# Kernel tuning notes

Hardware: AMD Instinct MI355X
Metric: run time of the kernel (lower is better)

The kernel has to match this reference:

```python
import jax, jax.numpy as jnp
import numpy as np


def setup_inputs() -> dict:
    key = jax.random.key(0)
    ks = jax.random.split(key, 6)
    B, C, S, E = 8, 16, 512, 256
    wscale = (2.0 / (E + E)) ** 0.5  # xavier_normal for [E, E] fan_in=fan_out=E
    return {
        "query": jax.random.normal(ks[0], (B, C, S, E), dtype=jnp.float32),
        "key": jax.random.normal(ks[1], (B, C, S, E), dtype=jnp.float32),
        "value": jax.random.normal(ks[2], (B, C, S, E), dtype=jnp.float32),
        "q_proj_weight": jax.random.normal(ks[3], (C, E, E), dtype=jnp.float32) * wscale,
        "k_proj_weight": jax.random.normal(ks[4], (C, E, E), dtype=jnp.float32) * wscale,
        "v_proj_weight": jax.random.normal(ks[5], (C, E, E), dtype=jnp.float32) * wscale,
        "q_proj_bias": jnp.zeros((C, 1, E), dtype=jnp.float32),
        "k_proj_bias": jnp.zeros((C, 1, E), dtype=jnp.float32),
        "v_proj_bias": jnp.zeros((C, 1, E), dtype=jnp.float32),
    }


def reference(query, key, value, q_proj_weight, k_proj_weight, v_proj_weight,
              q_proj_bias, k_proj_bias, v_proj_bias):
    E = query.shape[-1]
    # Per-cycle projection + bias + ReLU.  b=batch, c=cycle, s/t=seq, e/f=embed
    q = jax.nn.relu(jnp.einsum("bcse,cef->bcsf", query, q_proj_weight) + q_proj_bias)
    k = jax.nn.relu(jnp.einsum("bcse,cef->bcsf", key, k_proj_weight) + k_proj_bias)
    v = jax.nn.relu(jnp.einsum("bcse,cef->bcsf", value, v_proj_weight) + v_proj_bias)
    q = q * (float(E) ** -0.5)
    attn = jax.nn.softmax(jnp.einsum("bcse,bcte->bcst", q, k), axis=-1)
    out = jnp.einsum("bcst,bcte->bcse", attn, v)
    return out
```

## Files before the change

### kernel.cpp

```cpp
#include <hip/hip_runtime.h>

constexpr int BATCH = 8;
constexpr int CYC   = 16;
constexpr int SEQ   = 512;
constexpr int EMB   = 256;

typedef __attribute__((ext_vector_type(8))) short bf16x8;
typedef __attribute__((ext_vector_type(4))) float f32x4;

__device__ __forceinline__ unsigned short f2bf(float x) {
    unsigned int u = __float_as_uint(x);
    u += 0x7fffu + ((u >> 16) & 1u);
    return (unsigned short)(u >> 16);
}
__device__ __forceinline__ unsigned int pk2(float lo, float hi) {
    return (unsigned int)f2bf(lo) | ((unsigned int)f2bf(hi) << 16);
}

__device__ __forceinline__ f32x4 mfma16(bf16x8 a, bf16x8 b, f32x4 c) {
    return __builtin_amdgcn_mfma_f32_16x16x32_bf16(a, b, c, 0, 0, 0);
}

__device__ __forceinline__ void gll16(const unsigned short* g, unsigned short* l) {
    __builtin_amdgcn_global_load_lds(
        (const __attribute__((address_space(1))) void*)g,
        (__attribute__((address_space(3))) void*)l, 16, 0, 0);
}

__global__ __launch_bounds__(256) void wt_kernel(const float* __restrict__ W,
                                                 unsigned short* __restrict__ Wt) {
    __shared__ float tile[64][65];
    const int c  = blockIdx.z;
    const int e0 = blockIdx.x * 64;
    const int f0 = blockIdx.y * 64;
    const float* Wc = W + (size_t)c * EMB * EMB;
    unsigned short* Wtc = Wt + (size_t)c * EMB * EMB;
    const int t = threadIdx.x;
    {
        const int er = t >> 4;
        const int fc = (t & 15) * 4;
        for (int i = 0; i < 4; ++i) {
            const float4 v = *(const float4*)(Wc + (size_t)(e0 + er + i * 16) * EMB + f0 + fc);
            tile[er + i * 16][fc + 0] = v.x;
            tile[er + i * 16][fc + 1] = v.y;
            tile[er + i * 16][fc + 2] = v.z;
            tile[er + i * 16][fc + 3] = v.w;
        }
    }
    __syncthreads();
    {
        const int fr = t >> 4;
        const int ec = (t & 15) * 4;
        for (int i = 0; i < 4; ++i) {
            const int f = fr + i * 16;
            ushort4 o;
            o.x = f2bf(tile[ec + 0][f]);
            o.y = f2bf(tile[ec + 1][f]);
            o.z = f2bf(tile[ec + 2][f]);
            o.w = f2bf(tile[ec + 3][f]);
            *(ushort4*)(Wtc + (size_t)(f0 + f) * EMB + e0 + ec) = o;
        }
    }
}

__global__ __launch_bounds__(256) void proj_kernel(
    const float* __restrict__ X, const unsigned short* __restrict__ Wt,
    const float* __restrict__ bias, unsigned short* __restrict__ Y,
    const float scale, const int transposeOut)
{
    __shared__ unsigned short smem[10752];
    unsigned short* As = smem;
    unsigned short* Bs = smem + 2560;
    const int bc = blockIdx.x;
    const int c  = bc & (CYC - 1);
    const int m0 = blockIdx.y * 64;
    const float* Xb = X + (size_t)bc * SEQ * EMB;
    const unsigned short* Wc = Wt + (size_t)c * EMB * EMB;
    const float* bb = bias + (size_t)c * EMB;
    unsigned short* Yb = Y + (size_t)bc * SEQ * EMB;

    const int tid  = threadIdx.x;
    const int lane = tid & 63, w = tid >> 6;
    const int ln   = lane & 15, quad = lane >> 4;
    const int wu   = __builtin_amdgcn_readfirstlane(w);

    const int arow = tid >> 2;
    const int acol = (tid & 3) * 8;
    const int brow = lane >> 2;
    const int gch  = (lane & 3) ^ ((lane >> 3) & 3);
    const int bslot = quad ^ ((ln >> 1) & 3);

    f32x4 acc[4][4];
    for (int i = 0; i < 4; ++i)
        for (int j = 0; j < 4; ++j) acc[i][j] = (f32x4){0.f, 0.f, 0.f, 0.f};

    for (int kk = 0; kk < 8; ++kk) {
        const int k0 = kk * 32;
        const float* ax = Xb + (size_t)(m0 + arow) * EMB + k0 + acol;
        const float4 a0 = *(const float4*)ax;
        const float4 a1 = *(const float4*)(ax + 4);
        int4 pk;
        pk.x = pk2(a0.x, a0.y); pk.y = pk2(a0.z, a0.w);
        pk.z = pk2(a1.x, a1.y); pk.w = pk2(a1.z, a1.w);
        *(int4*)&As[arow * 40 + acol] = pk;
        for (int j = 0; j < 4; ++j) {
            const int r = wu * 64 + j * 16 + brow;
            gll16(Wc + (size_t)r * EMB + k0 + gch * 8,
                  Bs + (size_t)(wu * 64 + j * 16) * 32);
        }
        __syncthreads();
        bf16x8 af[4], bfv[4];
        for (int i = 0; i < 4; ++i)
            af[i] = *(const bf16x8*)&As[(i * 16 + ln) * 40 + quad * 8];
        for (int j = 0; j < 4; ++j)
            bfv[j] = *(const bf16x8*)&Bs[(w * 64 + j * 16 + ln) * 32 + bslot * 8];
        for (int i = 0; i < 4; ++i)
            for (int j = 0; j < 4; ++j)
                acc[i][j] = mfma16(af[i], bfv[j], acc[i][j]);
        __syncthreads();
    }

    float bvj[4];
    for (int j = 0; j < 4; ++j) bvj[j] = bb[w * 64 + j * 16 + ln];

    if (!transposeOut) {
        unsigned short* ep = smem + w * 1152;
        for (int i = 0; i < 4; ++i) {
            for (int j = 0; j < 4; ++j)
                for (int r = 0; r < 4; ++r)
                    ep[(quad * 4 + r) * 72 + j * 16 + ln] =
                        f2bf(fmaxf(acc[i][j][r] + bvj[j], 0.f) * scale);
            __syncthreads();
            for (int h = 0; h < 2; ++h) {
                const int cid = lane + h * 64;
                const int row = cid >> 3, ch = cid & 7;
                *(bf16x8*)&Yb[(size_t)(m0 + i * 16 + row) * EMB + w * 64 + ch * 8] =
                    *(const bf16x8*)&ep[row * 72 + ch * 8];
            }
            __syncthreads();
        }
    } else {
        for (int j = 0; j < 4; ++j) {
            const int fg = w * 64 + j * 16 + ln;
            for (int i = 0; i < 4; ++i) {
                const int mb = m0 + i * 16 + quad * 4;
                ushort4 u;
                u.x = f2bf(fmaxf(acc[i][j][0] + bvj[j], 0.f) * scale);
                u.y = f2bf(fmaxf(acc[i][j][1] + bvj[j], 0.f) * scale);
                u.z = f2bf(fmaxf(acc[i][j][2] + bvj[j], 0.f) * scale);
                u.w = f2bf(fmaxf(acc[i][j][3] + bvj[j], 0.f) * scale);
                *(ushort4*)&Yb[(size_t)fg * SEQ + mb] = u;
            }
        }
    }
}

__global__ __launch_bounds__(256) void attn_kernel(
    const unsigned short* __restrict__ Qp, const unsigned short* __restrict__ Kp,
    const unsigned short* __restrict__ Vt, float* __restrict__ Out)
{
    __shared__ unsigned short Ks[32][264];
    __shared__ unsigned short Vs[256][40];
    __shared__ unsigned short Ps[64][40];
    const int bc = blockIdx.x;
    const int qt = blockIdx.y;
    const unsigned short* Qb = Qp + (size_t)bc * SEQ * EMB;
    const unsigned short* Kb = Kp + (size_t)bc * SEQ * EMB;
    const unsigned short* Vb = Vt + (size_t)bc * SEQ * EMB;
    float* Ob = Out + (size_t)bc * SEQ * EMB;

    const int tid  = threadIdx.x;
    const int lane = tid & 63, w = tid >> 6;
    const int ln   = lane & 15, quad = lane >> 4;

    bf16x8 qf[8];
    const int qrow = qt * 64 + w * 16 + ln;
    for (int ke = 0; ke < 8; ++ke)
        qf[ke] = *(const bf16x8*)(Qb + (size_t)qrow * EMB + ke * 32 + quad * 8);

    f32x4 of[16];
    for (int n = 0; n < 16; ++n) of[n] = (f32x4){0.f, 0.f, 0.f, 0.f};
    float lsum[4] = {0.f, 0.f, 0.f, 0.f};

    for (int tt = 0; tt < 16; ++tt) {
        const int t0 = tt * 32;
        for (int i = 0; i < 4; ++i) {
            const int idx = tid + i * 256;
            const int r = idx >> 5, c8 = (idx & 31) * 8;
            *(bf16x8*)&Ks[r][c8] = *(const bf16x8*)(Kb + (size_t)(t0 + r) * EMB + c8);
        }
        for (int i = 0; i < 4; ++i) {
            const int idx = tid + i * 256;
            const int e = idx >> 2, c8 = (idx & 3) * 8;
            *(bf16x8*)&Vs[e][c8] = *(const bf16x8*)(Vb + (size_t)e * SEQ + t0 + c8);
        }
        __syncthreads();

        f32x4 sf0 = (f32x4){0.f,0.f,0.f,0.f}, sf1 = (f32x4){0.f,0.f,0.f,0.f};
        for (int ke = 0; ke < 8; ++ke) {
            bf16x8 b0 = *(const bf16x8*)&Ks[ln][ke * 32 + quad * 8];
            bf16x8 b1 = *(const bf16x8*)&Ks[16 + ln][ke * 32 + quad * 8];
            sf0 = mfma16(qf[ke], b0, sf0);
            sf1 = mfma16(qf[ke], b1, sf1);
        }

        float p0[4], p1[4];
        for (int r = 0; r < 4; ++r) {
            p0[r] = __expf(sf0[r]);
            p1[r] = __expf(sf1[r]);
            lsum[r] += p0[r] + p1[r];
        }
        for (int r = 0; r < 4; ++r) {
            Ps[w * 16 + quad * 4 + r][ln]      = f2bf(p0[r]);
            Ps[w * 16 + quad * 4 + r][16 + ln] = f2bf(p1[r]);
        }
        __syncthreads();

        bf16x8 af = *(const bf16x8*)&Ps[w * 16 + ln][quad * 8];
        for (int n = 0; n < 16; ++n) {
            bf16x8 bv = *(const bf16x8*)&Vs[n * 16 + ln][quad * 8];
            of[n] = mfma16(af, bv, of[n]);
        }
        __syncthreads();
    }

    for (int off = 1; off < 16; off <<= 1)
        for (int r = 0; r < 4; ++r)
            lsum[r] += __shfl_xor(lsum[r], off, 64);
    float inv[4];
    for (int r = 0; r < 4; ++r) inv[r] = 1.0f / lsum[r];
    const int mbase = qt * 64 + w * 16 + quad * 4;
    for (int n = 0; n < 16; ++n)
        for (int r = 0; r < 4; ++r)
            Ob[(size_t)(mbase + r) * EMB + n * 16 + ln] = of[n][r] * inv[r];
}

extern "C" void kernel_launch(void* const* d_in, const int* in_sizes, int n_in,
                              void* d_out, int out_size, void* d_ws, size_t ws_size,
                              hipStream_t stream) {
    const float* query = (const float*)d_in[0];
    const float* key_  = (const float*)d_in[1];
    const float* value = (const float*)d_in[2];
    const float* wq = (const float*)d_in[3];
    const float* wk = (const float*)d_in[4];
    const float* wv = (const float*)d_in[5];
    const float* bq = (const float*)d_in[6];
    const float* bk = (const float*)d_in[7];
    const float* bv = (const float*)d_in[8];
    float* out = (float*)d_out;

    char* ws = (char*)d_ws;
    const size_t wsz = (size_t)CYC * EMB * EMB * sizeof(unsigned short);
    const size_t psz = (size_t)BATCH * CYC * SEQ * EMB * sizeof(unsigned short);
    unsigned short* Wtq = (unsigned short*)(ws);
    unsigned short* Wtk = (unsigned short*)(ws + wsz);
    unsigned short* Wtv = (unsigned short*)(ws + 2 * wsz);
    unsigned short* Qp  = (unsigned short*)(ws + 3 * wsz);
    unsigned short* Kp  = (unsigned short*)(ws + 3 * wsz + psz);
    unsigned short* Vtp = (unsigned short*)(ws + 3 * wsz + 2 * psz);

    const dim3 tb(256);
    wt_kernel<<<dim3(4, 4, CYC), tb, 0, stream>>>(wq, Wtq);
    wt_kernel<<<dim3(4, 4, CYC), tb, 0, stream>>>(wk, Wtk);
    wt_kernel<<<dim3(4, 4, CYC), tb, 0, stream>>>(wv, Wtv);

    const dim3 pg(BATCH * CYC, SEQ / 64);
    proj_kernel<<<pg, tb, 0, stream>>>(query, Wtq, bq, Qp, 0.0625f, 0);
    proj_kernel<<<pg, tb, 0, stream>>>(key_,  Wtk, bk, Kp, 1.0f, 0);
    proj_kernel<<<pg, tb, 0, stream>>>(value, Wtv, bv, Vtp, 1.0f, 1);

    attn_kernel<<<dim3(BATCH * CYC, SEQ / 64), tb, 0, stream>>>(Qp, Kp, Vtp, out);
}
```

Before: 351.3 us.

## Merge Q/K/V launches, double-buffer LDS staging, read K directly in attention

The three weight-transpose launches and the three projection launches each become one launch, with blockIdx.z choosing among Q, K and V. The projection kernel now double-buffers fp32 activations and bf16 weights in LDS via async global-to-LDS loads and converts to bf16 after reading from LDS. The attention kernel drops the K tile from LDS and reads K fragments straight from global, while V tiles are double-buffered with async loads and explicit waitcnt/barriers. The aim is to cut launch overhead and hide load latency behind MFMA work, at the cost of more LDS per block and uncoalesced direct K reads.

Result: slower. 411.5 us (+17.1%).

```diff
diff --git a/kernel.cpp b/kernel.cpp
--- a/kernel.cpp
+++ b/kernel.cpp
@@ -16,21 +16,27 @@
 __device__ __forceinline__ unsigned int pk2(float lo, float hi) {
     return (unsigned int)f2bf(lo) | ((unsigned int)f2bf(hi) << 16);
 }
-
 __device__ __forceinline__ f32x4 mfma16(bf16x8 a, bf16x8 b, f32x4 c) {
     return __builtin_amdgcn_mfma_f32_16x16x32_bf16(a, b, c, 0, 0, 0);
 }
-
-__device__ __forceinline__ void gll16(const unsigned short* g, unsigned short* l) {
+__device__ __forceinline__ void gll16(const void* g, void* l) {
     __builtin_amdgcn_global_load_lds(
         (const __attribute__((address_space(1))) void*)g,
         (__attribute__((address_space(3))) void*)l, 16, 0, 0);
 }
-
-__global__ __launch_bounds__(256) void wt_kernel(const float* __restrict__ W,
-                                                 unsigned short* __restrict__ Wt) {
+union BCast { int4 i; bf16x8 v; };
+
+__global__ __launch_bounds__(256) void wt_kernel(
+    const float* __restrict__ Wq, const float* __restrict__ Wk,
+    const float* __restrict__ Wv,
+    unsigned short* __restrict__ Tq, unsigned short* __restrict__ Tk,
+    unsigned short* __restrict__ Tv)
+{
     __shared__ float tile[64][65];
-    const int c  = blockIdx.z;
+    const int z = blockIdx.z;
+    const int which = z >> 4, c = z & 15;
+    const float* W = which == 0 ? Wq : which == 1 ? Wk : Wv;
+    unsigned short* Wt = which == 0 ? Tq : which == 1 ? Tk : Tv;
     const int e0 = blockIdx.x * 64;
     const int f0 = blockIdx.y * 64;
     const float* Wc = W + (size_t)c * EMB * EMB;
@@ -63,14 +69,26 @@
     }
 }
 
-__global__ __launch_bounds__(256) void proj_kernel(
-    const float* __restrict__ X, const unsigned short* __restrict__ Wt,
-    const float* __restrict__ bias, unsigned short* __restrict__ Y,
-    const float scale, const int transposeOut)
+__global__ __launch_bounds__(256, 3) void proj_kernel(
+    const float* __restrict__ Xq, const float* __restrict__ Xk,
+    const float* __restrict__ Xv,
+    const unsigned short* __restrict__ Wq, const unsigned short* __restrict__ Wk,
+    const unsigned short* __restrict__ Wv,
+    const float* __restrict__ Bq, const float* __restrict__ Bk,
+    const float* __restrict__ Bv,
+    unsigned short* __restrict__ Yq, unsigned short* __restrict__ Yk,
+    unsigned short* __restrict__ Yv)
 {
-    __shared__ unsigned short smem[10752];
-    unsigned short* As = smem;
-    unsigned short* Bs = smem + 2560;
+    __shared__ float          As[2][64 * 32];
+    __shared__ unsigned short Bs[2][256 * 32];
+
+    const int z = blockIdx.z;
+    const float* X = z == 0 ? Xq : z == 1 ? Xk : Xv;
+    const unsigned short* Wt = z == 0 ? Wq : z == 1 ? Wk : Wv;
+    const float* bias = z == 0 ? Bq : z == 1 ? Bk : Bv;
+    unsigned short* Y = z == 0 ? Yq : z == 1 ? Yk : Yv;
+    const float scale = z == 0 ? 0.0625f : 1.0f;
+
     const int bc = blockIdx.x;
     const int c  = bc & (CYC - 1);
     const int m0 = blockIdx.y * 64;
@@ -84,47 +102,77 @@
     const int ln   = lane & 15, quad = lane >> 4;
     const int wu   = __builtin_amdgcn_readfirstlane(w);
 
-    const int arow = tid >> 2;
-    const int acol = (tid & 3) * 8;
+    const int arow = lane >> 3;
+    const int achk = (lane & 7) ^ arow;
     const int brow = lane >> 2;
     const int gch  = (lane & 3) ^ ((lane >> 3) & 3);
+    const int s8    = ln & 7;
     const int bslot = quad ^ ((ln >> 1) & 3);
 
     f32x4 acc[4][4];
     for (int i = 0; i < 4; ++i)
         for (int j = 0; j < 4; ++j) acc[i][j] = (f32x4){0.f, 0.f, 0.f, 0.f};
 
+    auto stage = [&](int kk, int b) {
+        const int k0 = kk * 32;
+#pragma unroll
+        for (int j = 0; j < 2; ++j) {
+            const int r0 = wu * 16 + j * 8;
+            gll16(Xb + (size_t)(m0 + r0 + arow) * EMB + k0 + achk * 4,
+                  &As[b][r0 * 32]);
+        }
+#pragma unroll
+        for (int j = 0; j < 4; ++j) {
+            const int r0 = wu * 64 + j * 16;
+            gll16(Wc + (size_t)(r0 + brow) * EMB + k0 + gch * 8,
+                  &Bs[b][r0 * 32]);
+        }
+    };
+
+    stage(0, 0);
+#pragma unroll
     for (int kk = 0; kk < 8; ++kk) {
-        const int k0 = kk * 32;
-        const float* ax = Xb + (size_t)(m0 + arow) * EMB + k0 + acol;
-        const float4 a0 = *(const float4*)ax;
-        const float4 a1 = *(const float4*)(ax + 4);
-        int4 pk;
-        pk.x = pk2(a0.x, a0.y); pk.y = pk2(a0.z, a0.w);
-        pk.z = pk2(a1.x, a1.y); pk.w = pk2(a1.z, a1.w);
-        *(int4*)&As[arow * 40 + acol] = pk;
-        for (int j = 0; j < 4; ++j) {
-            const int r = wu * 64 + j * 16 + brow;
-            gll16(Wc + (size_t)r * EMB + k0 + gch * 8,
-                  Bs + (size_t)(wu * 64 + j * 16) * 32);
-        }
-        __syncthreads();
+        const int cur = kk & 1;
+        if (kk < 7) {
+            stage(kk + 1, cur ^ 1);
+            asm volatile("s_waitcnt vmcnt(6)" ::: "memory");
+        } else {
+            asm volatile("s_waitcnt vmcnt(0)" ::: "memory");
+        }
+        __builtin_amdgcn_s_barrier();
+        __builtin_amdgcn_sched_barrier(0);
+
         bf16x8 af[4], bfv[4];
+#pragma unroll
+        for (int i = 0; i < 4; ++i) {
+            const float* ar = &As[cur][(i * 16 + ln) * 32];
+            const float4 f0 = *(const float4*)(ar + ((2 * quad)     ^ s8) * 4);
+            const float4 f1 = *(const float4*)(ar + ((2 * quad + 1) ^ s8) * 4);
+            BCast u;
+            u.i.x = pk2(f0.x, f0.y); u.i.y = pk2(f0.z, f0.w);
+            u.i.z = pk2(f1.x, f1.y); u.i.w = pk2(f1.z, f1.w);
+            af[i] = u.v;
+        }
+#pragma unroll
+        for (int j = 0; j < 4; ++j)
+            bfv[j] = *(const bf16x8*)&Bs[cur][(w * 64 + j * 16 + ln) * 32 + bslot * 8];
+#pragma unroll
         for (int i = 0; i < 4; ++i)
-            af[i] = *(const bf16x8*)&As[(i * 16 + ln) * 40 + quad * 8];
-        for (int j = 0; j < 4; ++j)
-            bfv[j] = *(const bf16x8*)&Bs[(w * 64 + j * 16 + ln) * 32 + bslot * 8];
-        for (int i = 0; i < 4; ++i)
+#pragma unroll
             for (int j = 0; j < 4; ++j)
                 acc[i][j] = mfma16(af[i], bfv[j], acc[i][j]);
-        __syncthreads();
+
+        __builtin_amdgcn_sched_barrier(0);
+        asm volatile("s_waitcnt lgkmcnt(0)" ::: "memory");
+        __builtin_amdgcn_s_barrier();
     }
 
     float bvj[4];
+#pragma unroll
     for (int j = 0; j < 4; ++j) bvj[j] = bb[w * 64 + j * 16 + ln];
 
-    if (!transposeOut) {
-        unsigned short* ep = smem + w * 1152;
+    if (z != 2) {
+        unsigned short* ep = (unsigned short*)&As[0][0] + w * 1152;
         for (int i = 0; i < 4; ++i) {
             for (int j = 0; j < 4; ++j)
                 for (int r = 0; r < 4; ++r)
@@ -155,12 +203,11 @@
     }
 }
 
-__global__ __launch_bounds__(256) void attn_kernel(
+__global__ __launch_bounds__(256, 3) void attn_kernel(
     const unsigned short* __restrict__ Qp, const unsigned short* __restrict__ Kp,
     const unsigned short* __restrict__ Vt, float* __restrict__ Out)
 {
-    __shared__ unsigned short Ks[32][264];
-    __shared__ unsigned short Vs[256][40];
+    __shared__ unsigned short Vs[2][256 * 32];
     __shared__ unsigned short Ps[64][40];
     const int bc = blockIdx.x;
     const int qt = blockIdx.y;
@@ -172,9 +219,14 @@
     const int tid  = threadIdx.x;
     const int lane = tid & 63, w = tid >> 6;
     const int ln   = lane & 15, quad = lane >> 4;
+    const int wu   = __builtin_amdgcn_readfirstlane(w);
+    const int brow = lane >> 2;
+    const int gch  = (lane & 3) ^ ((lane >> 3) & 3);
+    const int vslot = quad ^ ((ln >> 1) & 3);
 
     bf16x8 qf[8];
     const int qrow = qt * 64 + w * 16 + ln;
+#pragma unroll
     for (int ke = 0; ke < 8; ++ke)
         qf[ke] = *(const bf16x8*)(Qb + (size_t)qrow * EMB + ke * 32 + quad * 8);
 
@@ -182,46 +234,65 @@
     for (int n = 0; n < 16; ++n) of[n] = (f32x4){0.f, 0.f, 0.f, 0.f};
     float lsum[4] = {0.f, 0.f, 0.f, 0.f};
 
+    auto stageV = [&](int tt, int b) {
+        const int t0 = tt * 32;
+#pragma unroll
+        for (int j = 0; j < 4; ++j) {
+            const int r0 = wu * 64 + j * 16;
+            gll16(Vb + (size_t)(r0 + brow) * SEQ + t0 + gch * 8,
+                  &Vs[b][r0 * 32]);
+        }
+    };
+
+    stageV(0, 0);
+
+    const unsigned short* Kq = Kb + (size_t)ln * EMB + quad * 8;
+
     for (int tt = 0; tt < 16; ++tt) {
+        const int cur = tt & 1;
         const int t0 = tt * 32;
-        for (int i = 0; i < 4; ++i) {
-            const int idx = tid + i * 256;
-            const int r = idx >> 5, c8 = (idx & 31) * 8;
-            *(bf16x8*)&Ks[r][c8] = *(const bf16x8*)(Kb + (size_t)(t0 + r) * EMB + c8);
-        }
-        for (int i = 0; i < 4; ++i) {
-            const int idx = tid + i * 256;
-            const int e = idx >> 2, c8 = (idx & 3) * 8;
-            *(bf16x8*)&Vs[e][c8] = *(const bf16x8*)(Vb + (size_t)e * SEQ + t0 + c8);
-        }
-        __syncthreads();
 
         f32x4 sf0 = (f32x4){0.f,0.f,0.f,0.f}, sf1 = (f32x4){0.f,0.f,0.f,0.f};
+        const unsigned short* K0 = Kq + (size_t)t0 * EMB;
+#pragma unroll
         for (int ke = 0; ke < 8; ++ke) {
-            bf16x8 b0 = *(const bf16x8*)&Ks[ln][ke * 32 + quad * 8];
-            bf16x8 b1 = *(const bf16x8*)&Ks[16 + ln][ke * 32 + quad * 8];
+            bf16x8 b0 = *(const bf16x8*)(K0 + ke * 32);
+            bf16x8 b1 = *(const bf16x8*)(K0 + (size_t)16 * EMB + ke * 32);
             sf0 = mfma16(qf[ke], b0, sf0);
             sf1 = mfma16(qf[ke], b1, sf1);
         }
 
         float p0[4], p1[4];
+#pragma unroll
         for (int r = 0; r < 4; ++r) {
             p0[r] = __expf(sf0[r]);
             p1[r] = __expf(sf1[r]);
             lsum[r] += p0[r] + p1[r];
         }
+#pragma unroll
         for (int r = 0; r < 4; ++r) {
             Ps[w * 16 + quad * 4 + r][ln]      = f2bf(p0[r]);
             Ps[w * 16 + quad * 4 + r][16 + ln] = f2bf(p1[r]);
         }
-        __syncthreads();
+
+        if (tt < 15) {
+            stageV(tt + 1, cur ^ 1);
+            asm volatile("s_waitcnt vmcnt(4) lgkmcnt(0)" ::: "memory");
+        } else {
+            asm volatile("s_waitcnt vmcnt(0) lgkmcnt(0)" ::: "memory");
+        }
+        __builtin_amdgcn_s_barrier();
+        __builtin_amdgcn_sched_barrier(0);
 
         bf16x8 af = *(const bf16x8*)&Ps[w * 16 + ln][quad * 8];
+#pragma unroll
         for (int n = 0; n < 16; ++n) {
-            bf16x8 bv = *(const bf16x8*)&Vs[n * 16 + ln][quad * 8];
+            bf16x8 bv = *(const bf16x8*)&Vs[cur][(n * 16 + ln) * 32 + vslot * 8];
             of[n] = mfma16(af, bv, of[n]);
         }
-        __syncthreads();
+        __builtin_amdgcn_sched_barrier(0);
+        asm volatile("s_waitcnt lgkmcnt(0)" ::: "memory");
+        __builtin_amdgcn_s_barrier();
     }
 
     for (int off = 1; off < 16; off <<= 1)
@@ -260,14 +331,10 @@
     unsigned short* Vtp = (unsigned short*)(ws + 3 * wsz + 2 * psz);
 
     const dim3 tb(256);
-    wt_kernel<<<dim3(4, 4, CYC), tb, 0, stream>>>(wq, Wtq);
-    wt_kernel<<<dim3(4, 4, CYC), tb, 0, stream>>>(wk, Wtk);
-    wt_kernel<<<dim3(4, 4, CYC), tb, 0, stream>>>(wv, Wtv);
-
-    const dim3 pg(BATCH * CYC, SEQ / 64);
-    proj_kernel<<<pg, tb, 0, stream>>>(query, Wtq, bq, Qp, 0.0625f, 0);
-    proj_kernel<<<pg, tb, 0, stream>>>(key_,  Wtk, bk, Kp, 1.0f, 0);
-    proj_kernel<<<pg, tb, 0, stream>>>(value, Wtv, bv, Vtp, 1.0f, 1);
+    wt_kernel<<<dim3(4, 4, 3 * CYC), tb, 0, stream>>>(wq, wk, wv, Wtq, Wtk, Wtv);
+
+    proj_kernel<<<dim3(BATCH * CYC, SEQ / 64, 3), tb, 0, stream>>>(
+        query, key_, value, Wtq, Wtk, Wtv, bq, bk, bv, Qp, Kp, Vtp);
 
     attn_kernel<<<dim3(BATCH * CYC, SEQ / 64), tb, 0, stream>>>(Qp, Kp, Vtp, out);
 }
```
